# Performance work log

Measured on AMD Instinct MI355X. Metric: run time of the kernel, lower is better.

## Reference

```python
import jax, jax.numpy as jnp
import numpy as np

NUM_OBJ_CLS = 151  # VG object classes incl. background
C = NUM_OBJ_CLS - 1  # multi-hot width = 150
PATH_DIM = 1024
B, P = 128, 512  # images, pairs per image


def setup_inputs() -> dict:
    key = jax.random.key(0)
    k1, k2, k3 = jax.random.split(key, 3)
    # predicted object-class labels per image; foreground classes 1..150
    pair_preds = jax.random.randint(k1, (B, P), 1, NUM_OBJ_CLS)
    W = jax.random.normal(k2, (PATH_DIM, C), dtype=jnp.float32) * 0.02
    b = jax.random.normal(k3, (PATH_DIM,), dtype=jnp.float32) * 0.02
    return {"pair_preds": pair_preds, "W": W, "b": b}


def reference(pair_preds, W, b):
    # Per image, build a multi-hot over the 150 foreground classes:
    # tmp[:, p-1] = 1 for every predicted label p (set is idempotent, so
    # the np.unique in the original is immaterial). Every row of an image
    # shares the same multi-hot vector.
    Bq, Pq = pair_preds.shape
    cols = pair_preds - 1  # [B, P]
    multi_hot = jnp.zeros((Bq, C), dtype=jnp.float32)
    multi_hot = multi_hot.at[jnp.arange(Bq)[:, None], cols].set(1.0)  # [B, C]
    # Each image contributes pairs.shape[0] = P identical rows, concatenated.
    context = jnp.repeat(multi_hot, Pq, axis=0)  # [B*P, C]
    # Linear projection: [B*P, C] @ [C, D] + [D]
    return context @ W.T + b
```

## Files before the change

### kernel.cpp

```cpp
#include <hip/hip_runtime.h>

#define NB   128
#define NP   512
#define NC   150
#define ND   1024

__global__ __launch_bounds__(256) void compute_y_kernel(const int* __restrict__ preds,
                                                        const float* __restrict__ W,
                                                        const float* __restrict__ bias,
                                                        float* __restrict__ out) {
    __shared__ float sflag[NC];
    const unsigned bid  = blockIdx.x;
    const unsigned img  = bid >> 2;
    const unsigned dblk = bid & 3;
    const unsigned t    = threadIdx.x;

    if (t < NC) sflag[t] = 0.0f;
    __syncthreads();

    const int* pp = preds + (size_t)img * NP;
    #pragma unroll
    for (int p = (int)t; p < NP; p += 256) {
        int c = pp[p] - 1;
        sflag[c] = 1.0f;
    }
    __syncthreads();

    const int d = (int)(dblk * 256 + t);
    const float* w = W + (size_t)d * NC;
    float y = bias[d];
    #pragma unroll
    for (int c = 0; c < NC; ++c) {
        y += sflag[c] * w[c];
    }
    out[(size_t)img * NP * ND + (size_t)d] = y;
}

__global__ __launch_bounds__(256) void broadcast_kernel(const float4* src, float4* out) {
    const unsigned bid   = blockIdx.x;
    const unsigned img   = bid >> 3;
    const unsigned chunk = bid & 7;
    const unsigned t     = threadIdx.x;

    const size_t base = ((size_t)img << 17);
    const float4 v = src[base + t];

    unsigned p0 = chunk * 64;
    if (chunk == 0) p0 = 1;
    const unsigned p1 = chunk * 64 + 64;

    for (unsigned p = p0; p < p1; ++p) {
        out[base + ((size_t)p << 8) + t] = v;
    }
}

extern "C" void kernel_launch(void* const* d_in, const int* in_sizes, int n_in,
                              void* d_out, int out_size, void* d_ws, size_t ws_size,
                              hipStream_t stream) {
    const int*   preds = (const int*)d_in[0];
    const float* W     = (const float*)d_in[1];
    const float* bias  = (const float*)d_in[2];
    float*       out   = (float*)d_out;

    compute_y_kernel<<<dim3(NB * 4), dim3(256), 0, stream>>>(preds, W, bias, out);
    broadcast_kernel<<<dim3(NB * 8), dim3(256), 0, stream>>>((const float4*)out, (float4*)out);
}
```

Measured before the change: 60.11 us.

## Fuse projection and row broadcast into one kernel with nontemporal stores

```diff
diff --git a/kernel.cpp b/kernel.cpp
--- a/kernel.cpp
+++ b/kernel.cpp
@@ -4,53 +4,59 @@
 #define NP   512
 #define NC   150
 #define ND   1024
+#define ROWS 64
+#define CHUNKS (NP / ROWS)
 
-__global__ __launch_bounds__(256) void compute_y_kernel(const int* __restrict__ preds,
+typedef float  f4 __attribute__((ext_vector_type(4)));
+typedef float  f2 __attribute__((ext_vector_type(2)));
+typedef int    i4 __attribute__((ext_vector_type(4)));
+
+__global__ __launch_bounds__(256) void labellayer_fused(const int* __restrict__ preds,
                                                         const float* __restrict__ W,
                                                         const float* __restrict__ bias,
                                                         float* __restrict__ out) {
     __shared__ float sflag[NC];
-    const unsigned bid  = blockIdx.x;
-    const unsigned img  = bid >> 2;
-    const unsigned dblk = bid & 3;
-    const unsigned t    = threadIdx.x;
-
-    if (t < NC) sflag[t] = 0.0f;
-    __syncthreads();
-
-    const int* pp = preds + (size_t)img * NP;
-    #pragma unroll
-    for (int p = (int)t; p < NP; p += 256) {
-        int c = pp[p] - 1;
-        sflag[c] = 1.0f;
-    }
-    __syncthreads();
-
-    const int d = (int)(dblk * 256 + t);
-    const float* w = W + (size_t)d * NC;
-    float y = bias[d];
-    #pragma unroll
-    for (int c = 0; c < NC; ++c) {
-        y += sflag[c] * w[c];
-    }
-    out[(size_t)img * NP * ND + (size_t)d] = y;
-}
-
-__global__ __launch_bounds__(256) void broadcast_kernel(const float4* src, float4* out) {
     const unsigned bid   = blockIdx.x;
     const unsigned img   = bid >> 3;
     const unsigned chunk = bid & 7;
     const unsigned t     = threadIdx.x;
 
-    const size_t base = ((size_t)img << 17);
-    const float4 v = src[base + t];
+    if (t < NC) sflag[t] = 0.0f;
+    __syncthreads();
 
-    unsigned p0 = chunk * 64;
-    if (chunk == 0) p0 = 1;
-    const unsigned p1 = chunk * 64 + 64;
+    if (t < NP / 4) {
+        i4 c4 = ((const i4*)(preds + (size_t)img * NP))[t];
+        sflag[c4.x - 1] = 1.0f;
+        sflag[c4.y - 1] = 1.0f;
+        sflag[c4.z - 1] = 1.0f;
+        sflag[c4.w - 1] = 1.0f;
+    }
+    __syncthreads();
 
-    for (unsigned p = p0; p < p1; ++p) {
-        out[base + ((size_t)p << 8) + t] = v;
+    const f4 b4 = ((const f4*)bias)[t];
+    float s0 = b4.x, s1 = b4.y, s2 = b4.z, s3 = b4.w;
+    const f2* w0 = (const f2*)(W + (size_t)(4 * t + 0) * NC);
+    const f2* w1 = (const f2*)(W + (size_t)(4 * t + 1) * NC);
+    const f2* w2 = (const f2*)(W + (size_t)(4 * t + 2) * NC);
+    const f2* w3 = (const f2*)(W + (size_t)(4 * t + 3) * NC);
+    #pragma unroll 5
+    for (int j = 0; j < NC / 2; ++j) {
+        const float f0 = sflag[2 * j];
+        const float f1 = sflag[2 * j + 1];
+        const f2 a0 = w0[j], a1 = w1[j], a2 = w2[j], a3 = w3[j];
+        s0 += f0 * a0.x + f1 * a0.y;
+        s1 += f0 * a1.x + f1 * a1.y;
+        s2 += f0 * a2.x + f1 * a2.y;
+        s3 += f0 * a3.x + f1 * a3.y;
+    }
+    f4 v;
+    v.x = s0; v.y = s1; v.z = s2; v.w = s3;
+
+    f4* obase = (f4*)out + ((size_t)img << 17);
+    const unsigned p0 = chunk * ROWS;
+    #pragma unroll 4
+    for (unsigned p = p0; p < p0 + ROWS; ++p) {
+        __builtin_nontemporal_store(v, obase + ((size_t)p << 8) + t);
     }
 }
 
@@ -62,6 +68,5 @@
     const float* bias  = (const float*)d_in[2];
     float*       out   = (float*)d_out;
 
-    compute_y_kernel<<<dim3(NB * 4), dim3(256), 0, stream>>>(preds, W, bias, out);
-    broadcast_kernel<<<dim3(NB * 8), dim3(256), 0, stream>>>((const float4*)out, (float4*)out);
+    labellayer_fused<<<dim3(NB * CHUNKS), dim3(256), 0, stream>>>(preds, W, bias, out);
 }
```

Measured after the change: 191.0 us. 3.18x slower.
